# Kernel tuning notes

Measured on AMD Instinct MI355X. Metric: run time of the kernel, lower is better.

## Reference

```python
import jax, jax.numpy as jnp
import numpy as np
import math

D_MODEL = 1024
N_HEADS = 16
HEAD_DIM = D_MODEL // N_HEADS
SEQ_LEN = 8192
INCLUDE_LOCAL = 2


def get_dilated_positions(seq_len, include_local=2):
    # Faithful numpy port of the torch pattern generator (runs once at setup).
    max_attend = include_local + int(math.ceil(math.log2(seq_len + 1)))
    positions = np.zeros((seq_len, max_attend), dtype=np.int64)
    mask = np.zeros((seq_len, max_attend), dtype=bool)
    for i in range(seq_len):
        ap = [i]
        for j in range(1, include_local + 1):
            if i - j >= 0:
                ap.append(i - j)
        k = 2
        while i - 2 ** k >= 0:
            ap.append(i - 2 ** k)
            k += 1
        positions[i, :len(ap)] = ap
        mask[i, :len(ap)] = True
    return positions, mask


def setup_inputs() -> dict:
    key = jax.random.key(0)
    kx, kq, kk, kv, ko = jax.random.split(key, 5)
    x = jax.random.normal(kx, (1, SEQ_LEN, D_MODEL), dtype=jnp.float32)
    # nn.Linear(bias=False) weights, torch layout [out_features, in_features]
    s = 0.02
    q_w = jax.random.normal(kq, (D_MODEL, D_MODEL), dtype=jnp.float32) * s
    k_w = jax.random.normal(kk, (D_MODEL, D_MODEL), dtype=jnp.float32) * s
    v_w = jax.random.normal(kv, (D_MODEL, D_MODEL), dtype=jnp.float32) * s
    o_w = jax.random.normal(ko, (D_MODEL, D_MODEL), dtype=jnp.float32) * s
    pos_np, mask_np = get_dilated_positions(SEQ_LEN, INCLUDE_LOCAL)
    return {
        "x": x,
        "q_w": q_w, "k_w": k_w, "v_w": v_w, "o_w": o_w,
        "positions": jnp.asarray(pos_np),   # (S, A) int64 indices
        "attend_mask": jnp.asarray(mask_np) # (S, A) bool
    }


def reference(x, q_w, k_w, v_w, o_w, positions, attend_mask):
    B, S, _ = x.shape
    H, Dh = N_HEADS, HEAD_DIM
    scale = Dh ** -0.5

    q = (x @ q_w.T).reshape(B, S, H, Dh).transpose(0, 2, 1, 3)  # (B,H,S,Dh)
    k = (x @ k_w.T).reshape(B, S, H, Dh).transpose(0, 2, 1, 3)
    v = (x @ v_w.T).reshape(B, S, H, Dh).transpose(0, 2, 1, 3)

    # Gather K/V at the dilated positions: (B,H,S,A,Dh)
    k_sparse = k[:, :, positions, :]
    v_sparse = v[:, :, positions, :]

    scores = jnp.einsum('bhsd,bhsad->bhsa', q, k_sparse) * scale
    scores = jnp.where(attend_mask[None, None, :, :], scores, -jnp.inf)
    attn = jax.nn.softmax(scores, axis=-1)  # dropout p in eval / 0.0 -> identity

    out = jnp.einsum('bhsa,bhsad->bhsd', attn, v_sparse)
    out = out.transpose(0, 2, 1, 3).reshape(B, S, D_MODEL)
    return out @ o_w.T
```

## Files before the change

kernel.cpp:

```cpp
#include <hip/hip_runtime.h>
#include <hip/hip_bf16.h>

typedef __bf16 bf16_t;
typedef __bf16 bf16x4 __attribute__((ext_vector_type(4)));
typedef __bf16 bf16x8 __attribute__((ext_vector_type(8)));
typedef float floatx4 __attribute__((ext_vector_type(4)));

#define SEQ    8192
#define DM     1024
#define NHEADS 16
#define HDIM   64

__device__ __forceinline__ void async_ld16(bf16_t* lds, const bf16_t* g) {
  __builtin_amdgcn_global_load_lds(
      (__attribute__((address_space(1))) void*)g,
      (__attribute__((address_space(3))) void*)lds, 16, 0, 0);
}

__global__ __launch_bounds__(256)
void cvt_all(const float* __restrict__ x,  const float* __restrict__ qw,
             const float* __restrict__ kw, const float* __restrict__ vw,
             const float* __restrict__ ow,
             bf16_t* __restrict__ Xb,  bf16_t* __restrict__ QWb,
             bf16_t* __restrict__ KWb, bf16_t* __restrict__ VWb,
             bf16_t* __restrict__ OWb) {
  const int b = blockIdx.x;
  const float* in; bf16_t* out; int g;
  if (b < 8192) { in = x; out = Xb; g = b; }
  else {
    const int w  = (b - 8192) >> 10;
    const int wb = (b - 8192) & 1023;
    switch (w) {
      case 0:  in = qw; out = QWb; break;
      case 1:  in = kw; out = KWb; break;
      case 2:  in = vw; out = VWb; break;
      default: in = ow; out = OWb; break;
    }
    g = wb;
  }
  const int idx = (g * 256 + threadIdx.x) * 4;
  float4 v = *(const float4*)(in + idx);
  bf16x4 o = { (bf16_t)v.x, (bf16_t)v.y, (bf16_t)v.z, (bf16_t)v.w };
  *(bf16x4*)(out + idx) = o;
}

__global__ __launch_bounds__(256)
void gemm_qkv(const bf16_t* __restrict__ A,
              const bf16_t* __restrict__ Bq, const bf16_t* __restrict__ Bk,
              const bf16_t* __restrict__ Bv,
              bf16_t* __restrict__ Cq, bf16_t* __restrict__ Ck, bf16_t* __restrict__ Cv)
{
  const bf16_t* B = (blockIdx.z == 0) ? Bq : (blockIdx.z == 1) ? Bk : Bv;
  bf16_t*       C = (blockIdx.z == 0) ? Cq : (blockIdx.z == 1) ? Ck : Cv;
  constexpr int Kdim = DM;
  __shared__ __attribute__((aligned(16))) bf16_t sA[128 * 32];
  __shared__ __attribute__((aligned(16))) bf16_t sB[128 * 32];

  const int tid  = threadIdx.x;
  const int wave = tid >> 6;
  const int lane = tid & 63;
  const int quad = lane >> 4;
  const int r16  = lane & 15;
  const int wr   = (wave >> 1) * 64;
  const int wc   = (wave & 1) * 64;

  const size_t arow0 = (size_t)blockIdx.x * 128 + wave * 32 + (lane >> 2);
  const size_t brow0 = (size_t)blockIdx.y * 128 + wave * 32 + (lane >> 2);
  const bf16_t* Ag = A + arow0 * Kdim + (lane & 3) * 8;
  const bf16_t* Bg = B + brow0 * Kdim + (lane & 3) * 8;
  bf16_t* sAw = sA + wave * 32 * 32;
  bf16_t* sBw = sB + wave * 32 * 32;

  floatx4 acc[4][4];
  #pragma unroll
  for (int i = 0; i < 4; ++i)
    #pragma unroll
    for (int j = 0; j < 4; ++j)
      acc[i][j] = (floatx4)(0.0f);

  for (int ko = 0; ko < Kdim; ko += 32) {
    async_ld16(sAw,           Ag + ko);
    async_ld16(sAw + 16 * 32, Ag + 16 * Kdim + ko);
    async_ld16(sBw,           Bg + ko);
    async_ld16(sBw + 16 * 32, Bg + 16 * Kdim + ko);
    __syncthreads();

    bf16x8 af[4], bfr[4];
    #pragma unroll
    for (int mi = 0; mi < 4; ++mi)
      af[mi] = *(const bf16x8*)&sA[(wr + mi * 16 + r16) * 32 + quad * 8];
    #pragma unroll
    for (int ni = 0; ni < 4; ++ni)
      bfr[ni] = *(const bf16x8*)&sB[(wc + ni * 16 + r16) * 32 + quad * 8];

    #pragma unroll
    for (int mi = 0; mi < 4; ++mi)
      #pragma unroll
      for (int ni = 0; ni < 4; ++ni)
        acc[mi][ni] = __builtin_amdgcn_mfma_f32_16x16x32_bf16(af[mi], bfr[ni], acc[mi][ni], 0, 0, 0);

    __syncthreads();
  }

  const int crow0 = blockIdx.x * 128 + wr + quad * 4;
  const int ccol0 = blockIdx.y * 128 + wc + r16;
  #pragma unroll
  for (int mi = 0; mi < 4; ++mi)
    #pragma unroll
    for (int ni = 0; ni < 4; ++ni)
      #pragma unroll
      for (int r = 0; r < 4; ++r)
        C[(size_t)(crow0 + mi * 16 + r) * DM + (ccol0 + ni * 16)] = (bf16_t)acc[mi][ni][r];
}

__global__ __launch_bounds__(256)
void gemm_out(const bf16_t* __restrict__ A, const bf16_t* __restrict__ B,
              float* __restrict__ C)
{
  constexpr int Kdim = DM;
  __shared__ __attribute__((aligned(16))) bf16_t sA[128 * 32];
  __shared__ __attribute__((aligned(16))) bf16_t sB[64 * 32];

  const int tid  = threadIdx.x;
  const int wave = tid >> 6;
  const int lane = tid & 63;
  const int quad = lane >> 4;
  const int r16  = lane & 15;
  const int wr   = (wave >> 1) * 64;
  const int wc   = (wave & 1) * 32;

  const size_t arow = (size_t)blockIdx.x * 128 + wave * 32 + (lane >> 2);
  const size_t brow = (size_t)blockIdx.y * 64 + wave * 16 + (lane >> 2);
  const bf16_t* Ag = A + arow * Kdim + (lane & 3) * 8;
  const bf16_t* Bg = B + brow * Kdim + (lane & 3) * 8;
  bf16_t* sAw = sA + wave * 32 * 32;
  bf16_t* sBw = sB + wave * 16 * 32;

  floatx4 acc[4][2];
  #pragma unroll
  for (int i = 0; i < 4; ++i)
    #pragma unroll
    for (int j = 0; j < 2; ++j)
      acc[i][j] = (floatx4)(0.0f);

  for (int ko = 0; ko < Kdim; ko += 32) {
    async_ld16(sAw,           Ag + ko);
    async_ld16(sAw + 16 * 32, Ag + 16 * Kdim + ko);
    async_ld16(sBw,           Bg + ko);
    __syncthreads();

    bf16x8 af[4], bfr[2];
    #pragma unroll
    for (int mi = 0; mi < 4; ++mi)
      af[mi] = *(const bf16x8*)&sA[(wr + mi * 16 + r16) * 32 + quad * 8];
    #pragma unroll
    for (int ni = 0; ni < 2; ++ni)
      bfr[ni] = *(const bf16x8*)&sB[(wc + ni * 16 + r16) * 32 + quad * 8];

    #pragma unroll
    for (int mi = 0; mi < 4; ++mi)
      #pragma unroll
      for (int ni = 0; ni < 2; ++ni)
        acc[mi][ni] = __builtin_amdgcn_mfma_f32_16x16x32_bf16(af[mi], bfr[ni], acc[mi][ni], 0, 0, 0);

    __syncthreads();
  }

  const int crow0 = blockIdx.x * 128 + wr + quad * 4;
  const int ccol0 = blockIdx.y * 64 + wc + r16;
  #pragma unroll
  for (int mi = 0; mi < 4; ++mi)
    #pragma unroll
    for (int ni = 0; ni < 2; ++ni)
      #pragma unroll
      for (int r = 0; r < 4; ++r)
        C[(size_t)(crow0 + mi * 16 + r) * DM + (ccol0 + ni * 16)] = acc[mi][ni][r];
}

__global__ __launch_bounds__(256)
void dilated_attn(const bf16_t* __restrict__ Q, const bf16_t* __restrict__ K,
                  const bf16_t* __restrict__ V, bf16_t* O)
{
  const int lane = threadIdx.x & 63;
  const int qb   = (blockIdx.x & 7) * 256 + (blockIdx.x >> 3);
  const int i    = qb * 4 + (threadIdx.x >> 6);
  const size_t base = (size_t)i * DM + lane * 16;

  bf16x8 q0 = *(const bf16x8*)(Q + base);
  bf16x8 q1 = *(const bf16x8*)(Q + base + 8);
  float qf[16];
  #pragma unroll
  for (int j = 0; j < 8; ++j) { qf[j] = (float)q0[j] * 0.125f; qf[j + 8] = (float)q1[j] * 0.125f; }

  float m = -INFINITY, l = 0.0f;
  float acc[16];
  #pragma unroll
  for (int j = 0; j < 16; ++j) acc[j] = 0.0f;

  #pragma unroll
  for (int t = 0; t < 14; ++t) {
    const int offv  = (t == 0) ? 0 : (1 << (t - 1));
    const int pn    = i - offv;
    const bool valid = (pn >= 0);
    const size_t nb = (size_t)(valid ? pn : 0) * DM + lane * 16;
    bf16x8 k0 = *(const bf16x8*)(K + nb), k1 = *(const bf16x8*)(K + nb + 8);
    bf16x8 v0 = *(const bf16x8*)(V + nb), v1 = *(const bf16x8*)(V + nb + 8);

    float sc = 0.0f;
    #pragma unroll
    for (int j = 0; j < 8; ++j) sc += qf[j] * (float)k0[j] + qf[j + 8] * (float)k1[j];
    sc += __shfl_xor(sc, 1, 64);
    sc += __shfl_xor(sc, 2, 64);
    sc = valid ? sc : -INFINITY;

    float mn = fmaxf(m, sc);
    float co = __expf(m - mn);
    float w  = __expf(sc - mn);
    l = l * co + w;
    m = mn;
    #pragma unroll
    for (int j = 0; j < 8; ++j) {
      acc[j]     = acc[j]     * co + w * (float)v0[j];
      acc[j + 8] = acc[j + 8] * co + w * (float)v1[j];
    }
  }

  const float inv = 1.0f / l;
  bf16x8 o0, o1;
  #pragma unroll
  for (int j = 0; j < 8; ++j) { o0[j] = (bf16_t)(acc[j] * inv); o1[j] = (bf16_t)(acc[j + 8] * inv); }
  *(bf16x8*)(O + base)     = o0;
  *(bf16x8*)(O + base + 8) = o1;
}

extern "C" void kernel_launch(void* const* d_in, const int* in_sizes, int n_in,
                              void* d_out, int out_size, void* d_ws, size_t ws_size,
                              hipStream_t stream) {
  (void)in_sizes; (void)n_in; (void)out_size; (void)ws_size;
  const float* x  = (const float*)d_in[0];
  const float* qw = (const float*)d_in[1];
  const float* kw = (const float*)d_in[2];
  const float* vw = (const float*)d_in[3];
  const float* ow = (const float*)d_in[4];
  float* out = (float*)d_out;

  bf16_t* Xb  = (bf16_t*)d_ws;
  bf16_t* Qb  = Xb  + (size_t)SEQ * DM;
  bf16_t* Kb  = Qb  + (size_t)SEQ * DM;
  bf16_t* Vb  = Kb  + (size_t)SEQ * DM;
  bf16_t* QWb = Vb  + (size_t)SEQ * DM;
  bf16_t* KWb = QWb + (size_t)DM * DM;
  bf16_t* VWb = KWb + (size_t)DM * DM;
  bf16_t* OWb = VWb + (size_t)DM * DM;
  bf16_t* AO  = Qb;

  cvt_all<<<dim3(8192 + 4096), dim3(256), 0, stream>>>(x, qw, kw, vw, ow,
                                                       Xb, QWb, KWb, VWb, OWb);

  dim3 block(256);
  gemm_qkv<<<dim3(SEQ / 128, DM / 128, 3), block, 0, stream>>>(Xb, QWb, KWb, VWb, Qb, Kb, Vb);
  dilated_attn<<<dim3(SEQ / 4), block, 0, stream>>>(Qb, Kb, Vb, AO);
  gemm_out<<<dim3(SEQ / 128, DM / 64), block, 0, stream>>>(AO, OWb, out);
}
```

Measured before the change: 247.7 us.

## Double K-tile depth in QKV GEMM and software-pipeline dilated attention loads

The QKV GEMM now stages 64-wide K tiles in LDS instead of 32, halving the number of barrier pairs per block at the cost of doubled shared memory. The attention kernel replaces the fully unrolled 14-step loop over dilated offsets with a while loop that prefetches the next K/V row while computing the current one, and exits early for rows that have fewer valid neighbours. This skips masked out-of-range loads but brings in a data-dependent loop that may cause divergence across waves.

```diff
diff --git a/kernel.cpp b/kernel.cpp
--- a/kernel.cpp
+++ b/kernel.cpp
@@ -53,8 +53,8 @@
   const bf16_t* B = (blockIdx.z == 0) ? Bq : (blockIdx.z == 1) ? Bk : Bv;
   bf16_t*       C = (blockIdx.z == 0) ? Cq : (blockIdx.z == 1) ? Ck : Cv;
   constexpr int Kdim = DM;
-  __shared__ __attribute__((aligned(16))) bf16_t sA[128 * 32];
-  __shared__ __attribute__((aligned(16))) bf16_t sB[128 * 32];
+  __shared__ __attribute__((aligned(16))) bf16_t sA[128 * 64];
+  __shared__ __attribute__((aligned(16))) bf16_t sB[128 * 64];
 
   const int tid  = threadIdx.x;
   const int wave = tid >> 6;
@@ -64,12 +64,12 @@
   const int wr   = (wave >> 1) * 64;
   const int wc   = (wave & 1) * 64;
 
-  const size_t arow0 = (size_t)blockIdx.x * 128 + wave * 32 + (lane >> 2);
-  const size_t brow0 = (size_t)blockIdx.y * 128 + wave * 32 + (lane >> 2);
-  const bf16_t* Ag = A + arow0 * Kdim + (lane & 3) * 8;
-  const bf16_t* Bg = B + brow0 * Kdim + (lane & 3) * 8;
-  bf16_t* sAw = sA + wave * 32 * 32;
-  bf16_t* sBw = sB + wave * 32 * 32;
+  const size_t arow0 = (size_t)blockIdx.x * 128 + wave * 32 + (lane >> 3);
+  const size_t brow0 = (size_t)blockIdx.y * 128 + wave * 32 + (lane >> 3);
+  const bf16_t* Ag = A + arow0 * Kdim + (lane & 7) * 8;
+  const bf16_t* Bg = B + brow0 * Kdim + (lane & 7) * 8;
+  bf16_t* sAw = sA + wave * 32 * 64;
+  bf16_t* sBw = sB + wave * 32 * 64;
 
   floatx4 acc[4][4];
   #pragma unroll
@@ -78,26 +78,30 @@
     for (int j = 0; j < 4; ++j)
       acc[i][j] = (floatx4)(0.0f);
 
-  for (int ko = 0; ko < Kdim; ko += 32) {
-    async_ld16(sAw,           Ag + ko);
-    async_ld16(sAw + 16 * 32, Ag + 16 * Kdim + ko);
-    async_ld16(sBw,           Bg + ko);
-    async_ld16(sBw + 16 * 32, Bg + 16 * Kdim + ko);
-    __syncthreads();
-
-    bf16x8 af[4], bfr[4];
-    #pragma unroll
-    for (int mi = 0; mi < 4; ++mi)
-      af[mi] = *(const bf16x8*)&sA[(wr + mi * 16 + r16) * 32 + quad * 8];
-    #pragma unroll
-    for (int ni = 0; ni < 4; ++ni)
-      bfr[ni] = *(const bf16x8*)&sB[(wc + ni * 16 + r16) * 32 + quad * 8];
-
-    #pragma unroll
-    for (int mi = 0; mi < 4; ++mi)
+  for (int ko = 0; ko < Kdim; ko += 64) {
+    #pragma unroll
+    for (int n = 0; n < 4; ++n) {
+      async_ld16(sAw + n * 512, Ag + (size_t)n * 8 * Kdim + ko);
+      async_ld16(sBw + n * 512, Bg + (size_t)n * 8 * Kdim + ko);
+    }
+    __syncthreads();
+
+    #pragma unroll
+    for (int s = 0; s < 2; ++s) {
+      bf16x8 af[4], bfr[4];
+      #pragma unroll
+      for (int mi = 0; mi < 4; ++mi)
+        af[mi] = *(const bf16x8*)&sA[(wr + mi * 16 + r16) * 64 + s * 32 + quad * 8];
       #pragma unroll
       for (int ni = 0; ni < 4; ++ni)
-        acc[mi][ni] = __builtin_amdgcn_mfma_f32_16x16x32_bf16(af[mi], bfr[ni], acc[mi][ni], 0, 0, 0);
+        bfr[ni] = *(const bf16x8*)&sB[(wc + ni * 16 + r16) * 64 + s * 32 + quad * 8];
+
+      #pragma unroll
+      for (int mi = 0; mi < 4; ++mi)
+        #pragma unroll
+        for (int ni = 0; ni < 4; ++ni)
+          acc[mi][ni] = __builtin_amdgcn_mfma_f32_16x16x32_bf16(af[mi], bfr[ni], acc[mi][ni], 0, 0, 0);
+    }
 
     __syncthreads();
   }
@@ -197,21 +201,25 @@
   #pragma unroll
   for (int j = 0; j < 16; ++j) acc[j] = 0.0f;
 
-  #pragma unroll
-  for (int t = 0; t < 14; ++t) {
-    const int offv  = (t == 0) ? 0 : (1 << (t - 1));
-    const int pn    = i - offv;
-    const bool valid = (pn >= 0);
-    const size_t nb = (size_t)(valid ? pn : 0) * DM + lane * 16;
-    bf16x8 k0 = *(const bf16x8*)(K + nb), k1 = *(const bf16x8*)(K + nb + 8);
-    bf16x8 v0 = *(const bf16x8*)(V + nb), v1 = *(const bf16x8*)(V + nb + 8);
+  int off = 1;
+  bf16x8 k0 = *(const bf16x8*)(K + base), k1 = *(const bf16x8*)(K + base + 8);
+  bf16x8 v0 = *(const bf16x8*)(V + base), v1 = *(const bf16x8*)(V + base + 8);
+
+  while (true) {
+    const int pn = i - off;
+    const bool more = (pn >= 0);
+    bf16x8 nk0, nk1, nv0, nv1;
+    if (more) {
+      size_t nb = (size_t)pn * DM + lane * 16;
+      nk0 = *(const bf16x8*)(K + nb); nk1 = *(const bf16x8*)(K + nb + 8);
+      nv0 = *(const bf16x8*)(V + nb); nv1 = *(const bf16x8*)(V + nb + 8);
+    }
 
     float sc = 0.0f;
     #pragma unroll
     for (int j = 0; j < 8; ++j) sc += qf[j] * (float)k0[j] + qf[j + 8] * (float)k1[j];
     sc += __shfl_xor(sc, 1, 64);
     sc += __shfl_xor(sc, 2, 64);
-    sc = valid ? sc : -INFINITY;
 
     float mn = fmaxf(m, sc);
     float co = __expf(m - mn);
@@ -223,6 +231,10 @@
       acc[j]     = acc[j]     * co + w * (float)v0[j];
       acc[j + 8] = acc[j + 8] * co + w * (float)v1[j];
     }
+
+    if (!more) break;
+    k0 = nk0; k1 = nk1; v0 = nv0; v1 = nv1;
+    off <<= 1;
   }
 
   const float inv = 1.0f / l;
```

Result: faster. 240.8 us (-2.8%).

## Swizzle GEMM LDS layout, fold Q scale into GEMM, and loop attention with prefetch

Applied to the files above, without the earlier changes.

Both GEMMs now XOR-swizzle the 16-byte column chunk on the global-to-LDS load and on the fragment read, to cut LDS bank conflicts. The 1/sqrt(d) scale is applied in the Q projection epilogue and removed from the attention kernel. Attention switches from a fixed 14-step unrolled loop with masked loads to a data-dependent while loop that prefetches the next K/V row, so invalid positions are not loaded. The loop exits early for small i but is no longer fully unrolled, and it adds an extra bf16 rounding after the scale.

```diff
diff --git a/kernel.cpp b/kernel.cpp
--- a/kernel.cpp
+++ b/kernel.cpp
@@ -44,6 +44,7 @@
   *(bf16x4*)(out + idx) = o;
 }
 
+
 __global__ __launch_bounds__(256)
 void gemm_qkv(const bf16_t* __restrict__ A,
               const bf16_t* __restrict__ Bq, const bf16_t* __restrict__ Bk,
@@ -64,12 +65,15 @@
   const int wr   = (wave >> 1) * 64;
   const int wc   = (wave & 1) * 64;
 
+  const int gc = (lane & 3) ^ ((lane >> 3) & 3);
   const size_t arow0 = (size_t)blockIdx.x * 128 + wave * 32 + (lane >> 2);
   const size_t brow0 = (size_t)blockIdx.y * 128 + wave * 32 + (lane >> 2);
-  const bf16_t* Ag = A + arow0 * Kdim + (lane & 3) * 8;
-  const bf16_t* Bg = B + brow0 * Kdim + (lane & 3) * 8;
+  const bf16_t* Ag = A + arow0 * Kdim + gc * 8;
+  const bf16_t* Bg = B + brow0 * Kdim + gc * 8;
   bf16_t* sAw = sA + wave * 32 * 32;
   bf16_t* sBw = sB + wave * 32 * 32;
+
+  const int slotA = ((quad ^ ((r16 >> 1) & 3)) * 8);
 
   floatx4 acc[4][4];
   #pragma unroll
@@ -88,10 +92,10 @@
     bf16x8 af[4], bfr[4];
     #pragma unroll
     for (int mi = 0; mi < 4; ++mi)
-      af[mi] = *(const bf16x8*)&sA[(wr + mi * 16 + r16) * 32 + quad * 8];
+      af[mi] = *(const bf16x8*)&sA[(wr + mi * 16 + r16) * 32 + slotA];
     #pragma unroll
     for (int ni = 0; ni < 4; ++ni)
-      bfr[ni] = *(const bf16x8*)&sB[(wc + ni * 16 + r16) * 32 + quad * 8];
+      bfr[ni] = *(const bf16x8*)&sB[(wc + ni * 16 + r16) * 32 + slotA];
 
     #pragma unroll
     for (int mi = 0; mi < 4; ++mi)
@@ -102,6 +106,7 @@
     __syncthreads();
   }
 
+  const float scl = (blockIdx.z == 0) ? 0.125f : 1.0f;
   const int crow0 = blockIdx.x * 128 + wr + quad * 4;
   const int ccol0 = blockIdx.y * 128 + wc + r16;
   #pragma unroll
@@ -110,7 +115,7 @@
     for (int ni = 0; ni < 4; ++ni)
       #pragma unroll
       for (int r = 0; r < 4; ++r)
-        C[(size_t)(crow0 + mi * 16 + r) * DM + (ccol0 + ni * 16)] = (bf16_t)acc[mi][ni][r];
+        C[(size_t)(crow0 + mi * 16 + r) * DM + (ccol0 + ni * 16)] = (bf16_t)(acc[mi][ni][r] * scl);
 }
 
 __global__ __launch_bounds__(256)
@@ -129,12 +134,15 @@
   const int wr   = (wave >> 1) * 64;
   const int wc   = (wave & 1) * 32;
 
+  const int gc = (lane & 3) ^ ((lane >> 3) & 3);
   const size_t arow = (size_t)blockIdx.x * 128 + wave * 32 + (lane >> 2);
   const size_t brow = (size_t)blockIdx.y * 64 + wave * 16 + (lane >> 2);
-  const bf16_t* Ag = A + arow * Kdim + (lane & 3) * 8;
-  const bf16_t* Bg = B + brow * Kdim + (lane & 3) * 8;
+  const bf16_t* Ag = A + arow * Kdim + gc * 8;
+  const bf16_t* Bg = B + brow * Kdim + gc * 8;
   bf16_t* sAw = sA + wave * 32 * 32;
   bf16_t* sBw = sB + wave * 16 * 32;
+
+  const int slotA = ((quad ^ ((r16 >> 1) & 3)) * 8);
 
   floatx4 acc[4][2];
   #pragma unroll
@@ -152,10 +160,10 @@
     bf16x8 af[4], bfr[2];
     #pragma unroll
     for (int mi = 0; mi < 4; ++mi)
-      af[mi] = *(const bf16x8*)&sA[(wr + mi * 16 + r16) * 32 + quad * 8];
+      af[mi] = *(const bf16x8*)&sA[(wr + mi * 16 + r16) * 32 + slotA];
     #pragma unroll
     for (int ni = 0; ni < 2; ++ni)
-      bfr[ni] = *(const bf16x8*)&sB[(wc + ni * 16 + r16) * 32 + quad * 8];
+      bfr[ni] = *(const bf16x8*)&sB[(wc + ni * 16 + r16) * 32 + slotA];
 
     #pragma unroll
     for (int mi = 0; mi < 4; ++mi)
@@ -190,28 +198,32 @@
   bf16x8 q1 = *(const bf16x8*)(Q + base + 8);
   float qf[16];
   #pragma unroll
-  for (int j = 0; j < 8; ++j) { qf[j] = (float)q0[j] * 0.125f; qf[j + 8] = (float)q1[j] * 0.125f; }
+  for (int j = 0; j < 8; ++j) { qf[j] = (float)q0[j]; qf[j + 8] = (float)q1[j]; }
 
   float m = -INFINITY, l = 0.0f;
   float acc[16];
   #pragma unroll
   for (int j = 0; j < 16; ++j) acc[j] = 0.0f;
 
-  #pragma unroll
-  for (int t = 0; t < 14; ++t) {
-    const int offv  = (t == 0) ? 0 : (1 << (t - 1));
-    const int pn    = i - offv;
-    const bool valid = (pn >= 0);
-    const size_t nb = (size_t)(valid ? pn : 0) * DM + lane * 16;
-    bf16x8 k0 = *(const bf16x8*)(K + nb), k1 = *(const bf16x8*)(K + nb + 8);
-    bf16x8 v0 = *(const bf16x8*)(V + nb), v1 = *(const bf16x8*)(V + nb + 8);
+  int off = 1;
+  bf16x8 k0 = *(const bf16x8*)(K + base), k1 = *(const bf16x8*)(K + base + 8);
+  bf16x8 v0 = *(const bf16x8*)(V + base), v1 = *(const bf16x8*)(V + base + 8);
+
+  while (true) {
+    const int pn = i - off;
+    const bool more = (pn >= 0);
+    bf16x8 nk0, nk1, nv0, nv1;
+    if (more) {
+      size_t nb = (size_t)pn * DM + lane * 16;
+      nk0 = *(const bf16x8*)(K + nb); nk1 = *(const bf16x8*)(K + nb + 8);
+      nv0 = *(const bf16x8*)(V + nb); nv1 = *(const bf16x8*)(V + nb + 8);
+    }
 
     float sc = 0.0f;
     #pragma unroll
     for (int j = 0; j < 8; ++j) sc += qf[j] * (float)k0[j] + qf[j + 8] * (float)k1[j];
     sc += __shfl_xor(sc, 1, 64);
     sc += __shfl_xor(sc, 2, 64);
-    sc = valid ? sc : -INFINITY;
 
     float mn = fmaxf(m, sc);
     float co = __expf(m - mn);
@@ -223,6 +235,10 @@
       acc[j]     = acc[j]     * co + w * (float)v0[j];
       acc[j + 8] = acc[j + 8] * co + w * (float)v1[j];
     }
+
+    if (!more) break;
+    k0 = nk0; k1 = nk1; v0 = nv0; v1 = nv1;
+    off <<= 1;
   }
 
   const float inv = 1.0f / l;
```

Result: faster. 224.3 us (-9.5%).
